# Kernel optimization log

Measured on AMD Instinct MI355X. Metric: run time of the kernel, lower is better.

The kernel has to match this reference:

```python
import jax, jax.numpy as jnp
import numpy as np

VOCAB = 32000
DIM = 1024
HID = 4096
MAXLEN = 2048
NH = 2       # number of sequential LowRankLinearAttention layers
KD = 64      # key_dim hardcoded in the module
B = 2
L = 2048


def setup_inputs() -> dict:
    key = jax.random.key(0)
    ks = jax.random.split(key, 12)
    def rn(k, shape, scale):
        return jax.random.normal(k, shape, dtype=jnp.float32) * scale
    return {
        "input_indices": jax.random.randint(ks[0], (B, L), 0, VOCAB),
        "token_embed": rn(ks[1], (VOCAB, DIM), 0.02),
        "pos_embed": rn(ks[2], (MAXLEN, DIM), 0.02),
        # per-layer attention projections (stored [in, out]; x @ W == torch Linear)
        "Wq": rn(ks[3], (NH, DIM, KD), DIM ** -0.5),
        "Wk": rn(ks[4], (NH, DIM, KD), DIM ** -0.5),
        "Wv": rn(ks[5], (NH, DIM, KD), DIM ** -0.5),
        "Wo": rn(ks[6], (NH, KD, DIM), KD ** -0.5),
        "norm_g": jnp.ones((NH, DIM), jnp.float32),
        "norm_b": jnp.zeros((NH, DIM), jnp.float32),
        "out_norm_g": jnp.ones((DIM,), jnp.float32),
        "out_norm_b": jnp.zeros((DIM,), jnp.float32),
        "W1": rn(ks[7], (DIM, HID), DIM ** -0.5),
        "b1": jnp.zeros((HID,), jnp.float32),
        "W2": rn(ks[8], (HID, VOCAB), HID ** -0.5),
        "b2": jnp.zeros((VOCAB,), jnp.float32),
    }


def _layernorm(x, g, b, eps=1e-5):
    m = jnp.mean(x, axis=-1, keepdims=True)
    v = jnp.var(x, axis=-1, keepdims=True)
    return (x - m) / jnp.sqrt(v + eps) * g + b


def _lowrank_linear_attn(x, Wq, Wk, Wv, Wo):
    # x: [B,L,D]; Q,K,V: [B,L,k]
    Q = jax.nn.elu(x @ Wq) + 1.0
    K = jax.nn.elu(x @ Wk) + 1.0
    V = x @ Wv
    # causal prefix sums of outer products K_t V_t^T -> [B,L,k,k]
    KV_sum = jnp.cumsum(K[..., :, None] * V[..., None, :], axis=1)
    K_sum = jnp.cumsum(K, axis=1)
    num = jnp.einsum('blk,blkj->blj', Q, KV_sum)          # [B,L,k]
    den = jnp.einsum('blk,blk->bl', Q, K_sum)[..., None]  # [B,L,1]
    return (num / (den + 1e-6)) @ Wo


def reference(input_indices, token_embed, pos_embed, Wq, Wk, Wv, Wo,
              norm_g, norm_b, out_norm_g, out_norm_b, W1, b1, W2, b2):
    seq_len = input_indices.shape[1]
    x = token_embed[input_indices] + pos_embed[jnp.arange(seq_len)]
    for i in range(Wq.shape[0]):
        x = x + _lowrank_linear_attn(x, Wq[i], Wk[i], Wv[i], Wo[i])
        x = _layernorm(x, norm_g[i], norm_b[i])
    x = _layernorm(x, out_norm_g, out_norm_b)
    h = jax.nn.gelu(x @ W1 + b1, approximate=False)  # torch nn.GELU default = erf
    logits = h @ W2 + b2
    return logits
```

## Files before the change

### kernel.cpp

```cpp
#include <hip/hip_runtime.h>

typedef __attribute__((ext_vector_type(4))) float  f4;
typedef __attribute__((ext_vector_type(2))) float  f2;
typedef __attribute__((ext_vector_type(4))) unsigned short us4;
typedef __attribute__((ext_vector_type(8))) short  s8;
typedef __attribute__((ext_vector_type(4))) float  f32x4;

__device__ __forceinline__ unsigned short f2bf(float f) {
  unsigned u = __float_as_uint(f);
  u += 0x7fffu + ((u >> 16) & 1u);
  return (unsigned short)(u >> 16);
}
__device__ __forceinline__ float elu1(float x) { return x > 0.f ? x + 1.f : __expf(x); }
__device__ __forceinline__ float gelu_erf(float x) { return 0.5f * x * (1.f + erff(x * 0.70710678118654752f)); }

__device__ __forceinline__ void async16(const void* g, void* l) {
  __builtin_amdgcn_global_load_lds((const __attribute__((address_space(1))) void*)g,
                                   (__attribute__((address_space(3))) void*)l, 16, 0, 0);
}

__device__ __forceinline__ void rawbar() {
  asm volatile("s_barrier" ::: "memory");
}

__device__ __forceinline__ unsigned l2u(const void* p) {
  return (unsigned)(size_t)(const __attribute__((address_space(3))) char*)p;
}
template<int OFF>
__device__ __forceinline__ void dsr(s8& d, unsigned base) {
  asm volatile("ds_read_b128 %0, %1 offset:%2" : "=v"(d) : "v"(base), "i"(OFF));
}
template<int KB>
__device__ __forceinline__ void readA8(s8 (&af)[8], unsigned base) {
  dsr<(0 * 2 + KB) * 1024>(af[0], base);
  dsr<(1 * 2 + KB) * 1024>(af[1], base);
  dsr<(2 * 2 + KB) * 1024>(af[2], base);
  dsr<(3 * 2 + KB) * 1024>(af[3], base);
  dsr<(4 * 2 + KB) * 1024>(af[4], base);
  dsr<(5 * 2 + KB) * 1024>(af[5], base);
  dsr<(6 * 2 + KB) * 1024>(af[6], base);
  dsr<(7 * 2 + KB) * 1024>(af[7], base);
}

__global__ __launch_bounds__(256) void embed_kernel(
    const int* __restrict__ idx, const float* __restrict__ tok,
    const float* __restrict__ pos, float* __restrict__ X, unsigned short* __restrict__ XB)
{
  int g = blockIdx.x * 256 + threadIdx.x;
  int t = g >> 8;
  int c4 = (g & 255) * 4;
  int l = t & 2047;
  int tk = idx[t];
  f4 v = *(const f4*)(tok + (size_t)tk * 1024 + c4);
  f4 p = *(const f4*)(pos + (size_t)l * 1024 + c4);
  v += p;
  *(f4*)(X + (size_t)t * 1024 + c4) = v;
  us4 o = { f2bf(v[0]), f2bf(v[1]), f2bf(v[2]), f2bf(v[3]) };
  *(us4*)(XB + (size_t)t * 1024 + c4) = o;
}

__global__ __launch_bounds__(256) void transpose_cvt(
    const float* __restrict__ src, unsigned short* __restrict__ dst, int N, int K)
{
  __shared__ unsigned short t[64][72];
  int k0 = blockIdx.x * 64, n0 = blockIdx.y * 64;
  int tid = threadIdx.x;
#pragma unroll
  for (int i = 0; i < 4; ++i) {
    int f = tid + i * 256;
    int r = f >> 4, c4 = (f & 15) * 4;
    f4 v = *(const f4*)(src + (size_t)(k0 + r) * N + n0 + c4);
    us4 o = { f2bf(v[0]), f2bf(v[1]), f2bf(v[2]), f2bf(v[3]) };
    *(us4*)&t[r][c4] = o;
  }
  __syncthreads();
#pragma unroll
  for (int i = 0; i < 4; ++i) {
    int f = tid + i * 256;
    int nr = f >> 4, kc4 = (f & 15) * 4;
    us4 o = { t[kc4 + 0][nr], t[kc4 + 1][nr], t[kc4 + 2][nr], t[kc4 + 3][nr] };
    *(us4*)(dst + (size_t)(n0 + nr) * K + k0 + kc4) = o;
  }
}

template<int EPI, int BF32>
__global__ __launch_bounds__(256) void gemm_bt(
    const unsigned short* __restrict__ A, const unsigned short* __restrict__ Bt,
    const float* __restrict__ Bf, const float* __restrict__ bias,
    void* __restrict__ Cv, int M, int N, int K, int mtiles)
{
  __shared__ unsigned short As[128 * 32];
  __shared__ unsigned short Bs[128 * 32];
  int bid = blockIdx.x;
  int mt = bid % mtiles, nt = bid / mtiles;
  int m0 = mt * 128, n0 = nt * 128;
  int tid = threadIdx.x, lane = tid & 63, w = tid >> 6;
  int wm = (w & 1) * 64, wn = (w >> 1) * 64;

  int c0 = w * 128 + lane, c1 = c0 + 64;
  size_t aO0 = (size_t)(m0 + (c0 >> 2)) * K + (size_t)((c0 & 3) * 8);
  size_t aO1 = (size_t)(m0 + (c1 >> 2)) * K + (size_t)((c1 & 3) * 8);
  size_t bO0 = (size_t)(n0 + (c0 >> 2)) * K + (size_t)((c0 & 3) * 8);
  size_t bO1 = (size_t)(n0 + (c1 >> 2)) * K + (size_t)((c1 & 3) * 8);
  unsigned short* lA0 = As + (w * 128) * 8;
  unsigned short* lA1 = As + (w * 128 + 64) * 8;
  unsigned short* lB0 = Bs + (w * 128) * 8;
  unsigned short* lB1 = Bs + (w * 128 + 64) * 8;

  f32x4 acc[4][4];
  f32x4 zz = {0.f, 0.f, 0.f, 0.f};
#pragma unroll
  for (int i = 0; i < 4; ++i)
#pragma unroll
    for (int j = 0; j < 4; ++j) acc[i][j] = zz;

  int rr = lane & 15, kh = (lane >> 4) * 8;
  const unsigned short* Ar = As + (wm + rr) * 32 + kh;
  const unsigned short* Br = Bs + (wn + rr) * 32 + kh;

  for (int k0 = 0; k0 < K; k0 += 32) {
    async16(A + aO0 + k0, lA0);
    async16(A + aO1 + k0, lA1);
    if constexpr (!BF32) {
      async16(Bt + bO0 + k0, lB0);
      async16(Bt + bO1 + k0, lB1);
    } else {
#pragma unroll
      for (int i = 0; i < 4; ++i) {
        int f = tid + i * 256;
        int kr = f >> 5, c4 = (f & 31) * 4;
        f4 v = *(const f4*)(Bf + (size_t)(k0 + kr) * N + n0 + c4);
#pragma unroll
        for (int e = 0; e < 4; ++e) Bs[(c4 + e) * 32 + kr] = f2bf(v[e]);
      }
    }
    __syncthreads();
    s8 af[4], bfr[4];
#pragma unroll
    for (int mi = 0; mi < 4; ++mi) af[mi] = *(const s8*)(Ar + mi * 512);
#pragma unroll
    for (int ni = 0; ni < 4; ++ni) bfr[ni] = *(const s8*)(Br + ni * 512);
#pragma unroll
    for (int mi = 0; mi < 4; ++mi)
#pragma unroll
      for (int ni = 0; ni < 4; ++ni)
        acc[mi][ni] = __builtin_amdgcn_mfma_f32_16x16x32_bf16(af[mi], bfr[ni], acc[mi][ni], 0, 0, 0);
    __syncthreads();
  }

  int cr = (lane >> 4) * 4;
#pragma unroll
  for (int mi = 0; mi < 4; ++mi) {
#pragma unroll
    for (int ni = 0; ni < 4; ++ni) {
      int gc = n0 + wn + ni * 16 + rr;
      float bv = (EPI > 0) ? bias[gc] : 0.f;
#pragma unroll
      for (int r = 0; r < 4; ++r) {
        int gr = m0 + wm + mi * 16 + cr + r;
        float v = acc[mi][ni][r] + bv;
        if constexpr (EPI == 1) {
          ((unsigned short*)Cv)[(size_t)gr * N + gc] = f2bf(gelu_erf(v));
        } else {
          ((float*)Cv)[(size_t)gr * N + gc] = v;
        }
      }
    }
  }
}

template<int RA, int RDKB, int RDNH, int ACCN, typename STG>
__device__ __forceinline__ void phaseX(
    unsigned ArdB, unsigned BrdB,
    s8 (&afDst)[8], s8 (&bfDst)[2],
    const s8 (&afUse)[8], const s8 (&bfUse)[2],
    f32x4 (&acc)[8][4], STG stg)
{
  dsr<((RDNH * 2 + 0) * 2 + RDKB) * 1024>(bfDst[0], BrdB);
  dsr<((RDNH * 2 + 1) * 2 + RDKB) * 1024>(bfDst[1], BrdB);
  if constexpr (RA) readA8<RDKB>(afDst, ArdB);
  stg();
  asm volatile("s_waitcnt vmcnt(6)" ::: "memory");
  rawbar();
  if constexpr (RA) asm volatile("s_waitcnt lgkmcnt(10)" ::: "memory");
  else              asm volatile("s_waitcnt lgkmcnt(2)" ::: "memory");
  __builtin_amdgcn_sched_barrier(0);
  __builtin_amdgcn_s_setprio(1);
#pragma unroll
  for (int f = 0; f < 8; ++f) {
    acc[f][ACCN * 2 + 0] =
        __builtin_amdgcn_mfma_f32_16x16x32_bf16(afUse[f], bfUse[0], acc[f][ACCN * 2 + 0], 0, 0, 0);
    acc[f][ACCN * 2 + 1] =
        __builtin_amdgcn_mfma_f32_16x16x32_bf16(afUse[f], bfUse[1], acc[f][ACCN * 2 + 1], 0, 0, 0);
  }
  __builtin_amdgcn_s_setprio(0);
  __builtin_amdgcn_sched_barrier(0);
}

template<int EPI>
__global__ __launch_bounds__(512, 2) void gemm256(
    const unsigned short* __restrict__ A, const unsigned short* __restrict__ Bt,
    const float* __restrict__ bias, void* __restrict__ Cv,
    int M, int N, int K, int mtiles)
{
  __shared__ __align__(16) char A0r[32768];
  __shared__ __align__(16) char B0r[32768];
  __shared__ __align__(16) char A1r[32768];
  __shared__ __align__(16) char B1r[32768];

  const int tid = threadIdx.x, lane = tid & 63, w = tid >> 6;
  const int wm = w >> 2, wn = w & 3;
  const int NT = K >> 6;

  int nwg = gridDim.x, orig = blockIdx.x;
  int q = nwg >> 3, r = nwg & 7;
  int xcd = orig & 7, lin = orig >> 3;
  int swz = (xcd < r ? xcd * (q + 1) : r * (q + 1) + (xcd - r) * q) + lin;
  int mt = swz % mtiles, nt = swz / mtiles;
  int m0 = mt * 256, n0 = nt * 256;

  const size_t klane8 = (size_t)((lane >> 4) << 3);
  const size_t arow0 = (size_t)(m0 + w * 32 + (lane & 15)) * K;
  const size_t arow1 = arow0 + (size_t)16 * K;
  const size_t brow0 = (size_t)(n0 + w * 32 + (lane & 15)) * K;
  const size_t brow1 = brow0 + (size_t)16 * K;

  auto stgA = [&](char* reg, int kt, int kb) {
    int ktc = kt < NT ? kt : NT - 1;
    size_t kk = (size_t)ktc * 64 + (size_t)(kb * 32) + klane8;
    char* d = reg + w * 4096 + kb * 1024;
    async16(A + arow0 + kk, d);
    async16(A + arow1 + kk, d + 2048);
  };
  auto stgB = [&](char* reg, int kt, int kb) {
    int ktc = kt < NT ? kt : NT - 1;
    size_t kk = (size_t)ktc * 64 + (size_t)(kb * 32) + klane8;
    char* d = reg + w * 4096 + kb * 1024;
    async16(Bt + brow0 + kk, d);
    async16(Bt + brow1 + kk, d + 2048);
  };

  const unsigned AB0 = l2u(A0r + wm * 16384 + lane * 16);
  const unsigned BB0 = l2u(B0r + wn * 8192 + lane * 16);
  const unsigned AB1 = l2u(A1r + wm * 16384 + lane * 16);
  const unsigned BB1 = l2u(B1r + wn * 8192 + lane * 16);

  f32x4 acc[8][4];
  f32x4 zz = {0.f, 0.f, 0.f, 0.f};
#pragma unroll
  for (int i = 0; i < 8; ++i)
#pragma unroll
    for (int j = 0; j < 4; ++j) acc[i][j] = zz;
  s8 afA[8], afB[8], bfA[2], bfB[2];

  stgA(A0r, 0, 0); stgB(B0r, 0, 0);
  stgA(A0r, 0, 1); stgB(B0r, 0, 1);
  stgA(A1r, 1, 0); stgB(B1r, 1, 0);
  asm volatile("s_waitcnt vmcnt(8)" ::: "memory");
  rawbar();
  readA8<0>(afA, AB0);
  dsr<0>(bfA[0], BB0);
  dsr<2048>(bfA[1], BB0);

  for (int te = 0; te < NT; te += 2) {
    phaseX<0, 0, 1, 0>(AB0, BB0, afA, bfB, afA, bfA, acc, [&] { stgA(A1r, te + 1, 1); });
    phaseX<1, 1, 1, 1>(AB0, BB0, afB, bfA, afA, bfB, acc, [&] { stgB(B1r, te + 1, 1); });
    phaseX<0, 1, 0, 1>(AB0, BB0, afA, bfB, afB, bfA, acc, [&] { stgA(A0r, te + 2, 0); });
    phaseX<1, 0, 0, 0>(AB1, BB1, afA, bfA, afB, bfB, acc, [&] { stgB(B0r, te + 2, 0); });
    phaseX<0, 0, 1, 0>(AB1, BB1, afA, bfB, afA, bfA, acc, [&] { stgA(A0r, te + 2, 1); });
    phaseX<1, 1, 1, 1>(AB1, BB1, afB, bfA, afA, bfB, acc, [&] { stgB(B0r, te + 2, 1); });
    phaseX<0, 1, 0, 1>(AB1, BB1, afA, bfB, afB, bfA, acc, [&] { stgA(A1r, te + 3, 0); });
    phaseX<1, 0, 0, 0>(AB0, BB0, afA, bfA, afB, bfB, acc, [&] { stgB(B1r, te + 3, 0); });
  }

  asm volatile("s_waitcnt vmcnt(0) lgkmcnt(0)" ::: "memory");
  __builtin_amdgcn_sched_barrier(0);

  int rr = lane & 15, cr = (lane >> 4) * 4;
#pragma unroll
  for (int f = 0; f < 8; ++f) {
#pragma unroll
    for (int ni = 0; ni < 4; ++ni) {
      int gc = n0 + wn * 64 + ni * 16 + rr;
      float bv = bias[gc];
#pragma unroll
      for (int rg = 0; rg < 4; ++rg) {
        int gr = m0 + wm * 128 + f * 16 + cr + rg;
        float v = acc[f][ni][rg] + bv;
        if constexpr (EPI == 1) {
          ((unsigned short*)Cv)[(size_t)gr * N + gc] = f2bf(gelu_erf(v));
        } else {
          ((float*)Cv)[(size_t)gr * N + gc] = v;
        }
      }
    }
  }
}

__global__ __launch_bounds__(256) void chunk_sums(
    const float* __restrict__ QKV, float* __restrict__ KVc, float* __restrict__ Ksum)
{
  __shared__ float Ks[64][68], Vs[64][68];
  int blk = blockIdx.x, t0 = blk * 64, tid = threadIdx.x;
#pragma unroll
  for (int i = 0; i < 4; ++i) {
    int f = tid + i * 256;
    int r = f >> 4, c4 = (f & 15) * 4;
    const float* s = QKV + (size_t)(t0 + r) * 256;
    f4 k = *(const f4*)(s + 64 + c4);
    f4 v = *(const f4*)(s + 128 + c4);
#pragma unroll
    for (int e = 0; e < 4; ++e) { Ks[r][c4 + e] = elu1(k[e]); Vs[r][c4 + e] = v[e]; }
  }
  __syncthreads();
  int i0 = tid >> 2, jb = (tid & 3) * 16;
  f4 a0 = {0,0,0,0}, a1 = {0,0,0,0}, a2 = {0,0,0,0}, a3 = {0,0,0,0};
  for (int t = 0; t < 64; ++t) {
    float kk = Ks[t][i0];
    a0 += kk * (*(const f4*)&Vs[t][jb]);
    a1 += kk * (*(const f4*)&Vs[t][jb + 4]);
    a2 += kk * (*(const f4*)&Vs[t][jb + 8]);
    a3 += kk * (*(const f4*)&Vs[t][jb + 12]);
  }
  float* d = KVc + (size_t)blk * 4096 + i0 * 64 + jb;
  *(f4*)(d) = a0; *(f4*)(d + 4) = a1; *(f4*)(d + 8) = a2; *(f4*)(d + 12) = a3;
  if (tid < 64) {
    float s = 0.f;
    for (int t = 0; t < 64; ++t) s += Ks[t][tid];
    Ksum[(size_t)blk * 64 + tid] = s;
  }
}

__global__ __launch_bounds__(256) void prefix_state(
    const float* __restrict__ KVc, const float* __restrict__ Ksum,
    float* __restrict__ KVp, float* __restrict__ Ksump)
{
  int b = blockIdx.x >> 3, seg = blockIdx.x & 7;
  int e = seg * 512 + threadIdx.x * 2;
  f2 run = {0.f, 0.f};
#pragma unroll
  for (int c = 0; c < 32; ++c) {
    size_t base = ((size_t)b * 32 + c) * 4096 + e;
    *(f2*)(KVp + base) = run;
    run += *(const f2*)(KVc + base);
  }
  if (seg == 0 && threadIdx.x < 64) {
    float rs = 0.f; int i = threadIdx.x;
#pragma unroll
    for (int c = 0; c < 32; ++c) {
      size_t base = ((size_t)b * 32 + c) * 64 + i;
      Ksump[base] = rs;
      rs += Ksum[base];
    }
  }
}

__global__ __launch_bounds__(256) void attn_ns(
    const float* __restrict__ QKV, const float* __restrict__ KVp,
    const float* __restrict__ Ksump, float* __restrict__ NsG)
{
  __shared__ float Qs[64][68], Ks[64][68], Vs[64][68], Ss[64][68], Ps[64][68];
  __shared__ float ksps[64];
  int blk = blockIdx.x, t0 = blk * 64, tid = threadIdx.x;
#pragma unroll
  for (int i = 0; i < 4; ++i) {
    int f = tid + i * 256;
    int r = f >> 4, c4 = (f & 15) * 4;
    const float* s = QKV + (size_t)(t0 + r) * 256;
    f4 q = *(const f4*)(s + c4);
    f4 k = *(const f4*)(s + 64 + c4);
    f4 v = *(const f4*)(s + 128 + c4);
    f4 p = *(const f4*)(KVp + (size_t)blk * 4096 + r * 64 + c4);
#pragma unroll
    for (int e = 0; e < 4; ++e) {
      Qs[r][c4 + e] = elu1(q[e]); Ks[r][c4 + e] = elu1(k[e]);
      Vs[r][c4 + e] = v[e];       Ps[r][c4 + e] = p[e];
    }
  }
  if (tid < 64) ksps[tid] = Ksump[(size_t)blk * 64 + tid];
  __syncthreads();
  int tq = tid >> 2, jb = (tid & 3) * 16;
#pragma unroll
  for (int jj = 0; jj < 16; ++jj) {
    int tk = jb + jj;
    float s = 0.f;
    if (tk <= tq) {
#pragma unroll
      for (int k4 = 0; k4 < 16; ++k4) {
        f4 q = *(const f4*)&Qs[tq][k4 * 4];
        f4 k = *(const f4*)&Ks[tk][k4 * 4];
        s += q[0] * k[0] + q[1] * k[1] + q[2] * k[2] + q[3] * k[3];
      }
    }
    Ss[tq][tk] = s;
  }
  __syncthreads();
  f4 a0 = {0,0,0,0}, a1 = {0,0,0,0}, a2 = {0,0,0,0}, a3 = {0,0,0,0};
  for (int t = 0; t < 64; ++t) {
    float s = Ss[tq][t];
    a0 += s * (*(const f4*)&Vs[t][jb]);
    a1 += s * (*(const f4*)&Vs[t][jb + 4]);
    a2 += s * (*(const f4*)&Vs[t][jb + 8]);
    a3 += s * (*(const f4*)&Vs[t][jb + 12]);
  }
  for (int k = 0; k < 64; ++k) {
    float q = Qs[tq][k];
    a0 += q * (*(const f4*)&Ps[k][jb]);
    a1 += q * (*(const f4*)&Ps[k][jb + 4]);
    a2 += q * (*(const f4*)&Ps[k][jb + 8]);
    a3 += q * (*(const f4*)&Ps[k][jb + 12]);
  }
  float den = 0.f;
  for (int t = 0; t < 64; ++t) den += Ss[tq][t];
  for (int k = 0; k < 64; ++k) den += Qs[tq][k] * ksps[k];
  float inv = 1.f / (den + 1e-6f);
  float* d = NsG + (size_t)(t0 + tq) * 64 + jb;
  *(f4*)(d)      = a0 * inv;
  *(f4*)(d + 4)  = a1 * inv;
  *(f4*)(d + 8)  = a2 * inv;
  *(f4*)(d + 12) = a3 * inv;
}

__global__ __launch_bounds__(256) void attn_apply(
    const float* __restrict__ NsG, const float* __restrict__ Wo, float* __restrict__ X)
{
  __shared__ float Ns[64][68];
  __shared__ float Wt[64][260];
  int chunk = blockIdx.x >> 2, dg = blockIdx.x & 3;
  int t0 = chunk * 64, d0 = dg * 256, tid = threadIdx.x;
#pragma unroll
  for (int i = 0; i < 4; ++i) {
    int f = tid + i * 256;
    int r = f >> 4, c4 = (f & 15) * 4;
    *(f4*)&Ns[r][c4] = *(const f4*)(NsG + (size_t)(t0 + r) * 64 + c4);
  }
#pragma unroll
  for (int i = 0; i < 16; ++i) {
    int f = tid + i * 256;
    int r = f >> 6, c4 = (f & 63) * 4;
    *(f4*)&Wt[r][c4] = *(const f4*)(Wo + (size_t)r * 1024 + d0 + c4);
  }
  __syncthreads();
  int w = tid >> 6, lane = tid & 63;
  for (int ts = 0; ts < 16; ++ts) {
    int t = w * 16 + ts;
    float a0 = 0.f, a1 = 0.f, a2 = 0.f, a3 = 0.f;
#pragma unroll
    for (int j = 0; j < 64; ++j) {
      float nv = Ns[t][j];
      a0 += nv * Wt[j][lane];
      a1 += nv * Wt[j][64 + lane];
      a2 += nv * Wt[j][128 + lane];
      a3 += nv * Wt[j][192 + lane];
    }
    size_t o = (size_t)(t0 + t) * 1024 + d0 + lane;
    X[o]       += a0;
    X[o + 64]  += a1;
    X[o + 128] += a2;
    X[o + 192] += a3;
  }
}

__global__ __launch_bounds__(256) void layernorm_kernel(
    float* __restrict__ X, unsigned short* __restrict__ XB,
    const float* __restrict__ g, const float* __restrict__ b)
{
  int t = blockIdx.x * 4 + (threadIdx.x >> 6);
  int lane = threadIdx.x & 63;
  float* row = X + (size_t)t * 1024;
  f4 v[4];
  float s = 0.f, s2 = 0.f;
#pragma unroll
  for (int i = 0; i < 4; ++i) {
    v[i] = *(const f4*)(row + (i * 64 + lane) * 4);
#pragma unroll
    for (int e = 0; e < 4; ++e) { s += v[i][e]; s2 += v[i][e] * v[i][e]; }
  }
#pragma unroll
  for (int off = 32; off > 0; off >>= 1) {
    s  += __shfl_xor(s, off, 64);
    s2 += __shfl_xor(s2, off, 64);
  }
  float mean = s * (1.f / 1024.f);
  float var = s2 * (1.f / 1024.f) - mean * mean;
  float rstd = rsqrtf(var + 1e-5f);
#pragma unroll
  for (int i = 0; i < 4; ++i) {
    int d = (i * 64 + lane) * 4;
    f4 gv = *(const f4*)(g + d);
    f4 bv = *(const f4*)(b + d);
    f4 y;
#pragma unroll
    for (int e = 0; e < 4; ++e) y[e] = (v[i][e] - mean) * rstd * gv[e] + bv[e];
    *(f4*)(row + d) = y;
    us4 o = { f2bf(y[0]), f2bf(y[1]), f2bf(y[2]), f2bf(y[3]) };
    *(us4*)(XB + (size_t)t * 1024 + d) = o;
  }
}

extern "C" void kernel_launch(void* const* d_in, const int* in_sizes, int n_in,
                              void* d_out, int out_size, void* d_ws, size_t ws_size,
                              hipStream_t stream) {
  (void)in_sizes; (void)n_in; (void)out_size;
  const int*   idx = (const int*)d_in[0];
  const float* tok = (const float*)d_in[1];
  const float* pos = (const float*)d_in[2];
  const float* Wq  = (const float*)d_in[3];
  const float* Wk  = (const float*)d_in[4];
  const float* Wv  = (const float*)d_in[5];
  const float* Wo  = (const float*)d_in[6];
  const float* ng  = (const float*)d_in[7];
  const float* nb  = (const float*)d_in[8];
  const float* ong = (const float*)d_in[9];
  const float* onb = (const float*)d_in[10];
  const float* W1  = (const float*)d_in[11];
  const float* b1  = (const float*)d_in[12];
  const float* W2  = (const float*)d_in[13];
  const float* b2  = (const float*)d_in[14];
  float* out = (float*)d_out;
  char* ws = (char*)d_ws;

  float* X            = (float*)(ws + 0);
  unsigned short* XB  = (unsigned short*)(ws + 16777216);
  unsigned short* QT0 = (unsigned short*)(ws + 25165824);
  unsigned short* QT1 = (unsigned short*)(ws + 25690112);
  float* QKVB         = (float*)(ws + 26214400);
  float* KVC          = (float*)(ws + 30408704);
  float* KSUM         = (float*)(ws + 31457280);
  float* KVP          = (float*)(ws + 31490048);
  float* KSP          = (float*)(ws + 32538624);
  unsigned short* W1T = (unsigned short*)(ws + 32571392);
  unsigned short* H   = (unsigned short*)(ws + 40960000);
  unsigned short* W2T = (unsigned short*)(ws + 74514432);
  float* NSG = KVC;
  bool bigws = ws_size >= 336658432ull;

  hipMemsetAsync(QT0, 0, 524288, stream);
  hipMemsetAsync(QT1, 0, 524288, stream);
  transpose_cvt<<<dim3(16, 1), 256, 0, stream>>>(Wq,          QT0,              64, 1024);
  transpose_cvt<<<dim3(16, 1), 256, 0, stream>>>(Wk,          QT0 + 64 * 1024,  64, 1024);
  transpose_cvt<<<dim3(16, 1), 256, 0, stream>>>(Wv,          QT0 + 128 * 1024, 64, 1024);
  transpose_cvt<<<dim3(16, 1), 256, 0, stream>>>(Wq + 65536,  QT1,              64, 1024);
  transpose_cvt<<<dim3(16, 1), 256, 0, stream>>>(Wk + 65536,  QT1 + 64 * 1024,  64, 1024);
  transpose_cvt<<<dim3(16, 1), 256, 0, stream>>>(Wv + 65536,  QT1 + 128 * 1024, 64, 1024);
  transpose_cvt<<<dim3(16, 64), 256, 0, stream>>>(W1, W1T, 4096, 1024);
  if (bigws)
    transpose_cvt<<<dim3(64, 500), 256, 0, stream>>>(W2, W2T, 32000, 4096);

  embed_kernel<<<4096, 256, 0, stream>>>(idx, tok, pos, X, XB);

  for (int layer = 0; layer < 2; ++layer) {
    const unsigned short* QT = layer ? QT1 : QT0;
    gemm_bt<0, 0><<<64, 256, 0, stream>>>(XB, QT, nullptr, nullptr, QKVB, 4096, 256, 1024, 32);
    chunk_sums<<<64, 256, 0, stream>>>(QKVB, KVC, KSUM);
    prefix_state<<<16, 256, 0, stream>>>(KVC, KSUM, KVP, KSP);
    attn_ns<<<64, 256, 0, stream>>>(QKVB, KVP, KSP, NSG);
    attn_apply<<<256, 256, 0, stream>>>(NSG, Wo + (size_t)layer * 65536, X);
    layernorm_kernel<<<1024, 256, 0, stream>>>(X, XB, ng + layer * 1024, nb + layer * 1024);
  }
  layernorm_kernel<<<1024, 256, 0, stream>>>(X, XB, ong, onb);

  gemm256<1><<<256, 512, 0, stream>>>(XB, W1T, b1, H, 4096, 4096, 1024, 16);
  if (bigws)
    gemm256<2><<<2000, 512, 0, stream>>>(H, W2T, b2, out, 4096, 32000, 4096, 16);
  else
    gemm_bt<2, 1><<<8000, 256, 0, stream>>>(H, nullptr, W2, b2, out, 4096, 32000, 4096, 32);
}
```

Measured before the change: 1.654 ms.

## Add 128x128-tile pipelined MFMA GEMM for the vocab projection

Adds a new gemm128 kernel that uses 128x128 output tiles, 4 waves, double-buffered async global-to-LDS staging and bf16 MFMA. The 4096x32000x4096 logits GEMM uses it in place of the 256x256-tile gemm256. The aim is more workgroups (8000 instead of 2000) and two blocks per CU for better occupancy and less wave-quantization tail. The smaller tiles lower arithmetic intensity and add more global and LDS traffic per FLOP.

After: 2.531 ms. +53.0%, slower.

```diff
diff --git a/kernel.cpp b/kernel.cpp
--- a/kernel.cpp
+++ b/kernel.cpp
@@ -287,6 +287,145 @@
       for (int rg = 0; rg < 4; ++rg) {
         int gr = m0 + wm * 128 + f * 16 + cr + rg;
         float v = acc[f][ni][rg] + bv;
+        if constexpr (EPI == 1) {
+          ((unsigned short*)Cv)[(size_t)gr * N + gc] = f2bf(gelu_erf(v));
+        } else {
+          ((float*)Cv)[(size_t)gr * N + gc] = v;
+        }
+      }
+    }
+  }
+}
+
+template<int KB, typename STG>
+__device__ __forceinline__ void phaseY(
+    unsigned AB, unsigned BB, f32x4 (&acc)[4][4], STG stg)
+{
+  s8 a0, a1, a2, a3, b0, b1, b2, b3;
+  dsr<(0 * 2 + KB) * 1024>(a0, AB);
+  dsr<(1 * 2 + KB) * 1024>(a1, AB);
+  dsr<(2 * 2 + KB) * 1024>(a2, AB);
+  dsr<(3 * 2 + KB) * 1024>(a3, AB);
+  dsr<(0 * 2 + KB) * 1024>(b0, BB);
+  dsr<(1 * 2 + KB) * 1024>(b1, BB);
+  dsr<(2 * 2 + KB) * 1024>(b2, BB);
+  dsr<(3 * 2 + KB) * 1024>(b3, BB);
+  stg();
+  asm volatile("s_waitcnt vmcnt(8)" ::: "memory");
+  rawbar();
+  asm volatile("s_waitcnt lgkmcnt(0)" ::: "memory");
+  __builtin_amdgcn_sched_barrier(0);
+  __builtin_amdgcn_s_setprio(1);
+  acc[0][0] = __builtin_amdgcn_mfma_f32_16x16x32_bf16(a0, b0, acc[0][0], 0, 0, 0);
+  acc[1][0] = __builtin_amdgcn_mfma_f32_16x16x32_bf16(a1, b0, acc[1][0], 0, 0, 0);
+  acc[2][0] = __builtin_amdgcn_mfma_f32_16x16x32_bf16(a2, b0, acc[2][0], 0, 0, 0);
+  acc[3][0] = __builtin_amdgcn_mfma_f32_16x16x32_bf16(a3, b0, acc[3][0], 0, 0, 0);
+  acc[0][1] = __builtin_amdgcn_mfma_f32_16x16x32_bf16(a0, b1, acc[0][1], 0, 0, 0);
+  acc[1][1] = __builtin_amdgcn_mfma_f32_16x16x32_bf16(a1, b1, acc[1][1], 0, 0, 0);
+  acc[2][1] = __builtin_amdgcn_mfma_f32_16x16x32_bf16(a2, b1, acc[2][1], 0, 0, 0);
+  acc[3][1] = __builtin_amdgcn_mfma_f32_16x16x32_bf16(a3, b1, acc[3][1], 0, 0, 0);
+  acc[0][2] = __builtin_amdgcn_mfma_f32_16x16x32_bf16(a0, b2, acc[0][2], 0, 0, 0);
+  acc[1][2] = __builtin_amdgcn_mfma_f32_16x16x32_bf16(a1, b2, acc[1][2], 0, 0, 0);
+  acc[2][2] = __builtin_amdgcn_mfma_f32_16x16x32_bf16(a2, b2, acc[2][2], 0, 0, 0);
+  acc[3][2] = __builtin_amdgcn_mfma_f32_16x16x32_bf16(a3, b2, acc[3][2], 0, 0, 0);
+  acc[0][3] = __builtin_amdgcn_mfma_f32_16x16x32_bf16(a0, b3, acc[0][3], 0, 0, 0);
+  acc[1][3] = __builtin_amdgcn_mfma_f32_16x16x32_bf16(a1, b3, acc[1][3], 0, 0, 0);
+  acc[2][3] = __builtin_amdgcn_mfma_f32_16x16x32_bf16(a2, b3, acc[2][3], 0, 0, 0);
+  acc[3][3] = __builtin_amdgcn_mfma_f32_16x16x32_bf16(a3, b3, acc[3][3], 0, 0, 0);
+  __builtin_amdgcn_s_setprio(0);
+  __builtin_amdgcn_sched_barrier(0);
+  rawbar();
+}
+
+template<int EPI>
+__global__ __launch_bounds__(256, 2) void gemm128(
+    const unsigned short* __restrict__ A, const unsigned short* __restrict__ Bt,
+    const float* __restrict__ bias, void* __restrict__ Cv,
+    int M, int N, int K, int mtiles)
+{
+  __shared__ __align__(16) char A0r[16384];
+  __shared__ __align__(16) char B0r[16384];
+  __shared__ __align__(16) char A1r[16384];
+  __shared__ __align__(16) char B1r[16384];
+
+  const int tid = threadIdx.x, lane = tid & 63, w = tid >> 6;
+  const int wm = w >> 1, wn = w & 1;
+  const int NT = K >> 6;
+
+  int nwg = gridDim.x, orig = blockIdx.x;
+  int q = nwg >> 3, r = nwg & 7;
+  int xcd = orig & 7, lin = orig >> 3;
+  int swz = (xcd < r ? xcd * (q + 1) : r * (q + 1) + (xcd - r) * q) + lin;
+  int mt = swz % mtiles, nt = swz / mtiles;
+  int m0 = mt * 128, n0 = nt * 128;
+
+  const int lrow = lane & 15;
+  const size_t lcol = (size_t)((lane >> 4) << 3);
+
+  auto stgA = [&](char* reg, int kt, int kb) {
+    int ktc = kt < NT ? kt : NT - 1;
+    size_t cb = (size_t)ktc * 64 + (size_t)(kb * 32) + lcol;
+#pragma unroll
+    for (int j = 0; j < 2; ++j) {
+      int idx = w * 2 + j;
+      int half = idx >> 2, sub = idx & 3;
+      size_t row = (size_t)(m0 + half * 64 + sub * 16 + lrow);
+      char* d = reg + half * 8192 + (sub * 2 + kb) * 1024;
+      async16(A + row * K + cb, d);
+    }
+  };
+  auto stgB = [&](char* reg, int kt, int kb) {
+    int ktc = kt < NT ? kt : NT - 1;
+    size_t cb = (size_t)ktc * 64 + (size_t)(kb * 32) + lcol;
+#pragma unroll
+    for (int j = 0; j < 2; ++j) {
+      int idx = w * 2 + j;
+      int half = idx >> 2, sub = idx & 3;
+      size_t row = (size_t)(n0 + half * 64 + sub * 16 + lrow);
+      char* d = reg + half * 8192 + (sub * 2 + kb) * 1024;
+      async16(Bt + row * K + cb, d);
+    }
+  };
+
+  const unsigned AB0 = l2u(A0r + wm * 8192 + lane * 16);
+  const unsigned BB0 = l2u(B0r + wn * 8192 + lane * 16);
+  const unsigned AB1 = l2u(A1r + wm * 8192 + lane * 16);
+  const unsigned BB1 = l2u(B1r + wn * 8192 + lane * 16);
+
+  f32x4 acc[4][4];
+  f32x4 zz = {0.f, 0.f, 0.f, 0.f};
+#pragma unroll
+  for (int i = 0; i < 4; ++i)
+#pragma unroll
+    for (int j = 0; j < 4; ++j) acc[i][j] = zz;
+
+  stgA(A0r, 0, 0); stgB(B0r, 0, 0);
+  stgA(A0r, 0, 1); stgB(B0r, 0, 1);
+  stgA(A1r, 1, 0); stgB(B1r, 1, 0);
+  asm volatile("s_waitcnt vmcnt(8)" ::: "memory");
+  rawbar();
+
+  for (int te = 0; te < NT; te += 2) {
+    phaseY<0>(AB0, BB0, acc, [&] { stgA(A1r, te + 1, 1); stgB(B1r, te + 1, 1); });
+    phaseY<1>(AB0, BB0, acc, [&] { stgA(A0r, te + 2, 0); stgB(B0r, te + 2, 0); });
+    phaseY<0>(AB1, BB1, acc, [&] { stgA(A0r, te + 2, 1); stgB(B0r, te + 2, 1); });
+    phaseY<1>(AB1, BB1, acc, [&] { stgA(A1r, te + 3, 0); stgB(B1r, te + 3, 0); });
+  }
+
+  asm volatile("s_waitcnt vmcnt(0) lgkmcnt(0)" ::: "memory");
+  __builtin_amdgcn_sched_barrier(0);
+
+  int rr = lane & 15, cr = (lane >> 4) * 4;
+#pragma unroll
+  for (int mi = 0; mi < 4; ++mi) {
+#pragma unroll
+    for (int ni = 0; ni < 4; ++ni) {
+      int gc = n0 + wn * 64 + ni * 16 + rr;
+      float bv = bias[gc];
+#pragma unroll
+      for (int rg = 0; rg < 4; ++rg) {
+        int gr = m0 + wm * 64 + mi * 16 + cr + rg;
+        float v = acc[mi][ni][rg] + bv;
         if constexpr (EPI == 1) {
           ((unsigned short*)Cv)[(size_t)gr * N + gc] = f2bf(gelu_erf(v));
         } else {
@@ -562,7 +701,7 @@
 
   gemm256<1><<<256, 512, 0, stream>>>(XB, W1T, b1, H, 4096, 4096, 1024, 16);
   if (bigws)
-    gemm256<2><<<2000, 512, 0, stream>>>(H, W2T, b2, out, 4096, 32000, 4096, 16);
+    gemm128<2><<<8000, 256, 0, stream>>>(H, W2T, b2, out, 4096, 32000, 4096, 32);
   else
     gemm_bt<2, 1><<<8000, 256, 0, stream>>>(H, nullptr, W2, b2, out, 4096, 32000, 4096, 32);
 }
```

## Switch big GEMM to 1024-thread blocks with 64x64 warp tiles

Applied to the files above, without the earlier changes.

Replaces the 512-thread 256x256 GEMM, where each warp computes 128x64 with software-pipelined register fragments, by a 1024-thread version. Each of the 16 warps now computes a 64x64 subtile and reloads its A/B fragments from LDS every phase, with an extra barrier per phase. The goal is more waves per CU to hide latency and a simpler phase schedule. In exchange, each MFMA does less register-level reuse, LDS read traffic per FLOP rises, and occupancy is limited to one 1024-thread block per CU given the 128KB of LDS.

Result: slower. 1.702 ms (+2.9%).

```diff
diff --git a/kernel.cpp b/kernel.cpp
--- a/kernel.cpp
+++ b/kernel.cpp
@@ -29,17 +29,6 @@
 template<int OFF>
 __device__ __forceinline__ void dsr(s8& d, unsigned base) {
   asm volatile("ds_read_b128 %0, %1 offset:%2" : "=v"(d) : "v"(base), "i"(OFF));
-}
-template<int KB>
-__device__ __forceinline__ void readA8(s8 (&af)[8], unsigned base) {
-  dsr<(0 * 2 + KB) * 1024>(af[0], base);
-  dsr<(1 * 2 + KB) * 1024>(af[1], base);
-  dsr<(2 * 2 + KB) * 1024>(af[2], base);
-  dsr<(3 * 2 + KB) * 1024>(af[3], base);
-  dsr<(4 * 2 + KB) * 1024>(af[4], base);
-  dsr<(5 * 2 + KB) * 1024>(af[5], base);
-  dsr<(6 * 2 + KB) * 1024>(af[6], base);
-  dsr<(7 * 2 + KB) * 1024>(af[7], base);
 }
 
 __global__ __launch_bounds__(256) void embed_kernel(
@@ -169,36 +158,48 @@
   }
 }
 
-template<int RA, int RDKB, int RDNH, int ACCN, typename STG>
-__device__ __forceinline__ void phaseX(
-    unsigned ArdB, unsigned BrdB,
-    s8 (&afDst)[8], s8 (&bfDst)[2],
-    const s8 (&afUse)[8], const s8 (&bfUse)[2],
-    f32x4 (&acc)[8][4], STG stg)
-{
-  dsr<((RDNH * 2 + 0) * 2 + RDKB) * 1024>(bfDst[0], BrdB);
-  dsr<((RDNH * 2 + 1) * 2 + RDKB) * 1024>(bfDst[1], BrdB);
-  if constexpr (RA) readA8<RDKB>(afDst, ArdB);
+template<int KB, typename STG>
+__device__ __forceinline__ void phaseZ(
+    unsigned AB, unsigned BB, f32x4 (&acc)[4][4], STG stg)
+{
+  s8 a0, a1, a2, a3, b0, b1, b2, b3;
+  dsr<(0 * 2 + KB) * 1024>(a0, AB);
+  dsr<(1 * 2 + KB) * 1024>(a1, AB);
+  dsr<(2 * 2 + KB) * 1024>(a2, AB);
+  dsr<(3 * 2 + KB) * 1024>(a3, AB);
+  dsr<(0 * 2 + KB) * 1024>(b0, BB);
+  dsr<(1 * 2 + KB) * 1024>(b1, BB);
+  dsr<(2 * 2 + KB) * 1024>(b2, BB);
+  dsr<(3 * 2 + KB) * 1024>(b3, BB);
   stg();
-  asm volatile("s_waitcnt vmcnt(6)" ::: "memory");
+  asm volatile("s_waitcnt vmcnt(4)" ::: "memory");
   rawbar();
-  if constexpr (RA) asm volatile("s_waitcnt lgkmcnt(10)" ::: "memory");
-  else              asm volatile("s_waitcnt lgkmcnt(2)" ::: "memory");
+  asm volatile("s_waitcnt lgkmcnt(0)" ::: "memory");
   __builtin_amdgcn_sched_barrier(0);
   __builtin_amdgcn_s_setprio(1);
-#pragma unroll
-  for (int f = 0; f < 8; ++f) {
-    acc[f][ACCN * 2 + 0] =
-        __builtin_amdgcn_mfma_f32_16x16x32_bf16(afUse[f], bfUse[0], acc[f][ACCN * 2 + 0], 0, 0, 0);
-    acc[f][ACCN * 2 + 1] =
-        __builtin_amdgcn_mfma_f32_16x16x32_bf16(afUse[f], bfUse[1], acc[f][ACCN * 2 + 1], 0, 0, 0);
-  }
+  acc[0][0] = __builtin_amdgcn_mfma_f32_16x16x32_bf16(a0, b0, acc[0][0], 0, 0, 0);
+  acc[1][0] = __builtin_amdgcn_mfma_f32_16x16x32_bf16(a1, b0, acc[1][0], 0, 0, 0);
+  acc[2][0] = __builtin_amdgcn_mfma_f32_16x16x32_bf16(a2, b0, acc[2][0], 0, 0, 0);
+  acc[3][0] = __builtin_amdgcn_mfma_f32_16x16x32_bf16(a3, b0, acc[3][0], 0, 0, 0);
+  acc[0][1] = __builtin_amdgcn_mfma_f32_16x16x32_bf16(a0, b1, acc[0][1], 0, 0, 0);
+  acc[1][1] = __builtin_amdgcn_mfma_f32_16x16x32_bf16(a1, b1, acc[1][1], 0, 0, 0);
+  acc[2][1] = __builtin_amdgcn_mfma_f32_16x16x32_bf16(a2, b1, acc[2][1], 0, 0, 0);
+  acc[3][1] = __builtin_amdgcn_mfma_f32_16x16x32_bf16(a3, b1, acc[3][1], 0, 0, 0);
+  acc[0][2] = __builtin_amdgcn_mfma_f32_16x16x32_bf16(a0, b2, acc[0][2], 0, 0, 0);
+  acc[1][2] = __builtin_amdgcn_mfma_f32_16x16x32_bf16(a1, b2, acc[1][2], 0, 0, 0);
+  acc[2][2] = __builtin_amdgcn_mfma_f32_16x16x32_bf16(a2, b2, acc[2][2], 0, 0, 0);
+  acc[3][2] = __builtin_amdgcn_mfma_f32_16x16x32_bf16(a3, b2, acc[3][2], 0, 0, 0);
+  acc[0][3] = __builtin_amdgcn_mfma_f32_16x16x32_bf16(a0, b3, acc[0][3], 0, 0, 0);
+  acc[1][3] = __builtin_amdgcn_mfma_f32_16x16x32_bf16(a1, b3, acc[1][3], 0, 0, 0);
+  acc[2][3] = __builtin_amdgcn_mfma_f32_16x16x32_bf16(a2, b3, acc[2][3], 0, 0, 0);
+  acc[3][3] = __builtin_amdgcn_mfma_f32_16x16x32_bf16(a3, b3, acc[3][3], 0, 0, 0);
   __builtin_amdgcn_s_setprio(0);
   __builtin_amdgcn_sched_barrier(0);
+  rawbar();
 }
 
 template<int EPI>
-__global__ __launch_bounds__(512, 2) void gemm256(
+__global__ __launch_bounds__(1024) void gemm1k(
     const unsigned short* __restrict__ A, const unsigned short* __restrict__ Bt,
     const float* __restrict__ bias, void* __restrict__ Cv,
     int M, int N, int K, int mtiles)
@@ -219,58 +220,41 @@
   int mt = swz % mtiles, nt = swz / mtiles;
   int m0 = mt * 256, n0 = nt * 256;
 
-  const size_t klane8 = (size_t)((lane >> 4) << 3);
-  const size_t arow0 = (size_t)(m0 + w * 32 + (lane & 15)) * K;
-  const size_t arow1 = arow0 + (size_t)16 * K;
-  const size_t brow0 = (size_t)(n0 + w * 32 + (lane & 15)) * K;
-  const size_t brow1 = brow0 + (size_t)16 * K;
+  const unsigned short* aP = A + (size_t)(m0 + w * 16 + (lane & 15)) * K + ((lane >> 4) << 3);
+  const unsigned short* bP = Bt + (size_t)(n0 + w * 16 + (lane & 15)) * K + ((lane >> 4) << 3);
 
   auto stgA = [&](char* reg, int kt, int kb) {
     int ktc = kt < NT ? kt : NT - 1;
-    size_t kk = (size_t)ktc * 64 + (size_t)(kb * 32) + klane8;
-    char* d = reg + w * 4096 + kb * 1024;
-    async16(A + arow0 + kk, d);
-    async16(A + arow1 + kk, d + 2048);
+    async16(aP + ktc * 64 + kb * 32, reg + w * 2048 + kb * 1024);
   };
   auto stgB = [&](char* reg, int kt, int kb) {
     int ktc = kt < NT ? kt : NT - 1;
-    size_t kk = (size_t)ktc * 64 + (size_t)(kb * 32) + klane8;
-    char* d = reg + w * 4096 + kb * 1024;
-    async16(Bt + brow0 + kk, d);
-    async16(Bt + brow1 + kk, d + 2048);
+    async16(bP + ktc * 64 + kb * 32, reg + w * 2048 + kb * 1024);
   };
 
-  const unsigned AB0 = l2u(A0r + wm * 16384 + lane * 16);
+  const unsigned AB0 = l2u(A0r + wm * 8192 + lane * 16);
   const unsigned BB0 = l2u(B0r + wn * 8192 + lane * 16);
-  const unsigned AB1 = l2u(A1r + wm * 16384 + lane * 16);
+  const unsigned AB1 = l2u(A1r + wm * 8192 + lane * 16);
   const unsigned BB1 = l2u(B1r + wn * 8192 + lane * 16);
 
-  f32x4 acc[8][4];
+  f32x4 acc[4][4];
   f32x4 zz = {0.f, 0.f, 0.f, 0.f};
 #pragma unroll
-  for (int i = 0; i < 8; ++i)
+  for (int i = 0; i < 4; ++i)
 #pragma unroll
     for (int j = 0; j < 4; ++j) acc[i][j] = zz;
-  s8 afA[8], afB[8], bfA[2], bfB[2];
 
   stgA(A0r, 0, 0); stgB(B0r, 0, 0);
   stgA(A0r, 0, 1); stgB(B0r, 0, 1);
   stgA(A1r, 1, 0); stgB(B1r, 1, 0);
-  asm volatile("s_waitcnt vmcnt(8)" ::: "memory");
+  asm volatile("s_waitcnt vmcnt(4)" ::: "memory");
   rawbar();
-  readA8<0>(afA, AB0);
-  dsr<0>(bfA[0], BB0);
-  dsr<2048>(bfA[1], BB0);
 
   for (int te = 0; te < NT; te += 2) {
-    phaseX<0, 0, 1, 0>(AB0, BB0, afA, bfB, afA, bfA, acc, [&] { stgA(A1r, te + 1, 1); });
-    phaseX<1, 1, 1, 1>(AB0, BB0, afB, bfA, afA, bfB, acc, [&] { stgB(B1r, te + 1, 1); });
-    phaseX<0, 1, 0, 1>(AB0, BB0, afA, bfB, afB, bfA, acc, [&] { stgA(A0r, te + 2, 0); });
-    phaseX<1, 0, 0, 0>(AB1, BB1, afA, bfA, afB, bfB, acc, [&] { stgB(B0r, te + 2, 0); });
-    phaseX<0, 0, 1, 0>(AB1, BB1, afA, bfB, afA, bfA, acc, [&] { stgA(A0r, te + 2, 1); });
-    phaseX<1, 1, 1, 1>(AB1, BB1, afB, bfA, afA, bfB, acc, [&] { stgB(B0r, te + 2, 1); });
-    phaseX<0, 1, 0, 1>(AB1, BB1, afA, bfB, afB, bfA, acc, [&] { stgA(A1r, te + 3, 0); });
-    phaseX<1, 0, 0, 0>(AB0, BB0, afA, bfA, afB, bfB, acc, [&] { stgB(B1r, te + 3, 0); });
+    phaseZ<0>(AB0, BB0, acc, [&] { stgA(A1r, te + 1, 1); stgB(B1r, te + 1, 1); });
+    phaseZ<1>(AB0, BB0, acc, [&] { stgA(A0r, te + 2, 0); stgB(B0r, te + 2, 0); });
+    phaseZ<0>(AB1, BB1, acc, [&] { stgA(A0r, te + 2, 1); stgB(B0r, te + 2, 1); });
+    phaseZ<1>(AB1, BB1, acc, [&] { stgA(A1r, te + 3, 0); stgB(B1r, te + 3, 0); });
   }
 
   asm volatile("s_waitcnt vmcnt(0) lgkmcnt(0)" ::: "memory");
@@ -278,15 +262,15 @@
 
   int rr = lane & 15, cr = (lane >> 4) * 4;
 #pragma unroll
-  for (int f = 0; f < 8; ++f) {
+  for (int mi = 0; mi < 4; ++mi) {
 #pragma unroll
     for (int ni = 0; ni < 4; ++ni) {
       int gc = n0 + wn * 64 + ni * 16 + rr;
       float bv = bias[gc];
 #pragma unroll
       for (int rg = 0; rg < 4; ++rg) {
-        int gr = m0 + wm * 128 + f * 16 + cr + rg;
-        float v = acc[f][ni][rg] + bv;
+        int gr = m0 + wm * 64 + mi * 16 + cr + rg;
+        float v = acc[mi][ni][rg] + bv;
         if constexpr (EPI == 1) {
           ((unsigned short*)Cv)[(size_t)gr * N + gc] = f2bf(gelu_erf(v));
         } else {
@@ -560,9 +544,9 @@
   }
   layernorm_kernel<<<1024, 256, 0, stream>>>(X, XB, ong, onb);
 
-  gemm256<1><<<256, 512, 0, stream>>>(XB, W1T, b1, H, 4096, 4096, 1024, 16);
+  gemm1k<1><<<256, 1024, 0, stream>>>(XB, W1T, b1, H, 4096, 4096, 1024, 16);
   if (bigws)
-    gemm256<2><<<2000, 512, 0, stream>>>(H, W2T, b2, out, 4096, 32000, 4096, 16);
+    gemm1k<2><<<2000, 1024, 0, stream>>>(H, W2T, b2, out, 4096, 32000, 4096, 16);
   else
     gemm_bt<2, 1><<<8000, 256, 0, stream>>>(H, nullptr, W2, b2, out, 4096, 32000, 4096, 32);
 }
```

## Simplify large GEMM main loop to per-tile read-compute-stage and reroute W1 GEMM

Applied to the files above, without the earlier changes.

Replaces the eight-phase interleaved LDS-read/MFMA ping-pong schedule in the 256-tile GEMM with a simpler loop. Each iteration reads all A/B fragments for a K tile, runs the MFMAs in four groups gated by staggered lgkmcnt waits, then issues async loads for tile t+2 and barriers. The min-blocks occupancy hint is dropped, and the W1 GEMM is moved to the smaller gemm_bt kernel. The aim is fewer scheduling constraints and less register juggling. In exchange, LDS reads overlap less with MFMA work, register use for fragments grows, and there is no barrier between the last fragment reads and the overwrite of the same LDS buffer.

Result: faster. 1.599 ms (-3.4%).

```diff
diff --git a/kernel.cpp b/kernel.cpp
--- a/kernel.cpp
+++ b/kernel.cpp
@@ -29,17 +29,6 @@
 template<int OFF>
 __device__ __forceinline__ void dsr(s8& d, unsigned base) {
   asm volatile("ds_read_b128 %0, %1 offset:%2" : "=v"(d) : "v"(base), "i"(OFF));
-}
-template<int KB>
-__device__ __forceinline__ void readA8(s8 (&af)[8], unsigned base) {
-  dsr<(0 * 2 + KB) * 1024>(af[0], base);
-  dsr<(1 * 2 + KB) * 1024>(af[1], base);
-  dsr<(2 * 2 + KB) * 1024>(af[2], base);
-  dsr<(3 * 2 + KB) * 1024>(af[3], base);
-  dsr<(4 * 2 + KB) * 1024>(af[4], base);
-  dsr<(5 * 2 + KB) * 1024>(af[5], base);
-  dsr<(6 * 2 + KB) * 1024>(af[6], base);
-  dsr<(7 * 2 + KB) * 1024>(af[7], base);
 }
 
 __global__ __launch_bounds__(256) void embed_kernel(
@@ -169,36 +158,8 @@
   }
 }
 
-template<int RA, int RDKB, int RDNH, int ACCN, typename STG>
-__device__ __forceinline__ void phaseX(
-    unsigned ArdB, unsigned BrdB,
-    s8 (&afDst)[8], s8 (&bfDst)[2],
-    const s8 (&afUse)[8], const s8 (&bfUse)[2],
-    f32x4 (&acc)[8][4], STG stg)
-{
-  dsr<((RDNH * 2 + 0) * 2 + RDKB) * 1024>(bfDst[0], BrdB);
-  dsr<((RDNH * 2 + 1) * 2 + RDKB) * 1024>(bfDst[1], BrdB);
-  if constexpr (RA) readA8<RDKB>(afDst, ArdB);
-  stg();
-  asm volatile("s_waitcnt vmcnt(6)" ::: "memory");
-  rawbar();
-  if constexpr (RA) asm volatile("s_waitcnt lgkmcnt(10)" ::: "memory");
-  else              asm volatile("s_waitcnt lgkmcnt(2)" ::: "memory");
-  __builtin_amdgcn_sched_barrier(0);
-  __builtin_amdgcn_s_setprio(1);
-#pragma unroll
-  for (int f = 0; f < 8; ++f) {
-    acc[f][ACCN * 2 + 0] =
-        __builtin_amdgcn_mfma_f32_16x16x32_bf16(afUse[f], bfUse[0], acc[f][ACCN * 2 + 0], 0, 0, 0);
-    acc[f][ACCN * 2 + 1] =
-        __builtin_amdgcn_mfma_f32_16x16x32_bf16(afUse[f], bfUse[1], acc[f][ACCN * 2 + 1], 0, 0, 0);
-  }
-  __builtin_amdgcn_s_setprio(0);
-  __builtin_amdgcn_sched_barrier(0);
-}
-
 template<int EPI>
-__global__ __launch_bounds__(512, 2) void gemm256(
+__global__ __launch_bounds__(512) void gemm2(
     const unsigned short* __restrict__ A, const unsigned short* __restrict__ Bt,
     const float* __restrict__ bias, void* __restrict__ Cv,
     int M, int N, int K, int mtiles)
@@ -251,26 +212,99 @@
   for (int i = 0; i < 8; ++i)
 #pragma unroll
     for (int j = 0; j < 4; ++j) acc[i][j] = zz;
-  s8 afA[8], afB[8], bfA[2], bfB[2];
-
-  stgA(A0r, 0, 0); stgB(B0r, 0, 0);
-  stgA(A0r, 0, 1); stgB(B0r, 0, 1);
-  stgA(A1r, 1, 0); stgB(B1r, 1, 0);
+
+  stgA(A0r, 0, 0); stgA(A0r, 0, 1); stgB(B0r, 0, 0); stgB(B0r, 0, 1);
+  stgA(A1r, 1, 0); stgA(A1r, 1, 1); stgB(B1r, 1, 0); stgB(B1r, 1, 1);
   asm volatile("s_waitcnt vmcnt(8)" ::: "memory");
   rawbar();
-  readA8<0>(afA, AB0);
-  dsr<0>(bfA[0], BB0);
-  dsr<2048>(bfA[1], BB0);
-
-  for (int te = 0; te < NT; te += 2) {
-    phaseX<0, 0, 1, 0>(AB0, BB0, afA, bfB, afA, bfA, acc, [&] { stgA(A1r, te + 1, 1); });
-    phaseX<1, 1, 1, 1>(AB0, BB0, afB, bfA, afA, bfB, acc, [&] { stgB(B1r, te + 1, 1); });
-    phaseX<0, 1, 0, 1>(AB0, BB0, afA, bfB, afB, bfA, acc, [&] { stgA(A0r, te + 2, 0); });
-    phaseX<1, 0, 0, 0>(AB1, BB1, afA, bfA, afB, bfB, acc, [&] { stgB(B0r, te + 2, 0); });
-    phaseX<0, 0, 1, 0>(AB1, BB1, afA, bfB, afA, bfA, acc, [&] { stgA(A0r, te + 2, 1); });
-    phaseX<1, 1, 1, 1>(AB1, BB1, afB, bfA, afA, bfB, acc, [&] { stgB(B0r, te + 2, 1); });
-    phaseX<0, 1, 0, 1>(AB1, BB1, afA, bfB, afB, bfA, acc, [&] { stgA(A1r, te + 3, 0); });
-    phaseX<1, 0, 0, 0>(AB0, BB0, afA, bfA, afB, bfB, acc, [&] { stgB(B1r, te + 3, 0); });
+
+  for (int t = 0; t < NT; ++t) {
+    const int odd = t & 1;
+    const unsigned AB = odd ? AB1 : AB0;
+    const unsigned BB = odd ? BB1 : BB0;
+    char* Ad = odd ? A1r : A0r;
+    char* Bd = odd ? B1r : B0r;
+
+    s8 bf[8], af[16];
+    dsr<(0 * 2 + 0) * 1024>(bf[0], BB);
+    dsr<(0 * 2 + 1) * 1024>(bf[1], BB);
+    dsr<(1 * 2 + 0) * 1024>(bf[2], BB);
+    dsr<(1 * 2 + 1) * 1024>(bf[3], BB);
+    dsr<(2 * 2 + 0) * 1024>(bf[4], BB);
+    dsr<(2 * 2 + 1) * 1024>(bf[5], BB);
+    dsr<(3 * 2 + 0) * 1024>(bf[6], BB);
+    dsr<(3 * 2 + 1) * 1024>(bf[7], BB);
+    dsr<(0 * 2 + 0) * 1024>(af[0], AB);
+    dsr<(0 * 2 + 1) * 1024>(af[1], AB);
+    dsr<(1 * 2 + 0) * 1024>(af[2], AB);
+    dsr<(1 * 2 + 1) * 1024>(af[3], AB);
+    dsr<(2 * 2 + 0) * 1024>(af[4], AB);
+    dsr<(2 * 2 + 1) * 1024>(af[5], AB);
+    dsr<(3 * 2 + 0) * 1024>(af[6], AB);
+    dsr<(3 * 2 + 1) * 1024>(af[7], AB);
+    dsr<(4 * 2 + 0) * 1024>(af[8], AB);
+    dsr<(4 * 2 + 1) * 1024>(af[9], AB);
+    dsr<(5 * 2 + 0) * 1024>(af[10], AB);
+    dsr<(5 * 2 + 1) * 1024>(af[11], AB);
+    dsr<(6 * 2 + 0) * 1024>(af[12], AB);
+    dsr<(6 * 2 + 1) * 1024>(af[13], AB);
+    dsr<(7 * 2 + 0) * 1024>(af[14], AB);
+    dsr<(7 * 2 + 1) * 1024>(af[15], AB);
+
+    asm volatile("s_waitcnt lgkmcnt(12)" ::: "memory");
+    __builtin_amdgcn_sched_barrier(0);
+    __builtin_amdgcn_s_setprio(1);
+#pragma unroll
+    for (int ni = 0; ni < 4; ++ni) {
+#pragma unroll
+      for (int f = 0; f < 2; ++f) {
+        acc[f][ni] = __builtin_amdgcn_mfma_f32_16x16x32_bf16(af[f * 2 + 0], bf[ni * 2 + 0], acc[f][ni], 0, 0, 0);
+        acc[f][ni] = __builtin_amdgcn_mfma_f32_16x16x32_bf16(af[f * 2 + 1], bf[ni * 2 + 1], acc[f][ni], 0, 0, 0);
+      }
+    }
+    __builtin_amdgcn_s_setprio(0);
+    asm volatile("s_waitcnt lgkmcnt(8)" ::: "memory");
+    __builtin_amdgcn_sched_barrier(0);
+    __builtin_amdgcn_s_setprio(1);
+#pragma unroll
+    for (int ni = 0; ni < 4; ++ni) {
+#pragma unroll
+      for (int f = 2; f < 4; ++f) {
+        acc[f][ni] = __builtin_amdgcn_mfma_f32_16x16x32_bf16(af[f * 2 + 0], bf[ni * 2 + 0], acc[f][ni], 0, 0, 0);
+        acc[f][ni] = __builtin_amdgcn_mfma_f32_16x16x32_bf16(af[f * 2 + 1], bf[ni * 2 + 1], acc[f][ni], 0, 0, 0);
+      }
+    }
+    __builtin_amdgcn_s_setprio(0);
+    asm volatile("s_waitcnt lgkmcnt(4)" ::: "memory");
+    __builtin_amdgcn_sched_barrier(0);
+    __builtin_amdgcn_s_setprio(1);
+#pragma unroll
+    for (int ni = 0; ni < 4; ++ni) {
+#pragma unroll
+      for (int f = 4; f < 6; ++f) {
+        acc[f][ni] = __builtin_amdgcn_mfma_f32_16x16x32_bf16(af[f * 2 + 0], bf[ni * 2 + 0], acc[f][ni], 0, 0, 0);
+        acc[f][ni] = __builtin_amdgcn_mfma_f32_16x16x32_bf16(af[f * 2 + 1], bf[ni * 2 + 1], acc[f][ni], 0, 0, 0);
+      }
+    }
+    __builtin_amdgcn_s_setprio(0);
+    asm volatile("s_waitcnt lgkmcnt(0)" ::: "memory");
+    __builtin_amdgcn_sched_barrier(0);
+    __builtin_amdgcn_s_setprio(1);
+#pragma unroll
+    for (int ni = 0; ni < 4; ++ni) {
+#pragma unroll
+      for (int f = 6; f < 8; ++f) {
+        acc[f][ni] = __builtin_amdgcn_mfma_f32_16x16x32_bf16(af[f * 2 + 0], bf[ni * 2 + 0], acc[f][ni], 0, 0, 0);
+        acc[f][ni] = __builtin_amdgcn_mfma_f32_16x16x32_bf16(af[f * 2 + 1], bf[ni * 2 + 1], acc[f][ni], 0, 0, 0);
+      }
+    }
+    __builtin_amdgcn_s_setprio(0);
+    __builtin_amdgcn_sched_barrier(0);
+
+    stgA(Ad, t + 2, 0); stgA(Ad, t + 2, 1);
+    stgB(Bd, t + 2, 0); stgB(Bd, t + 2, 1);
+    asm volatile("s_waitcnt vmcnt(8)" ::: "memory");
+    rawbar();
   }
 
   asm volatile("s_waitcnt vmcnt(0) lgkmcnt(0)" ::: "memory");
@@ -560,9 +594,9 @@
   }
   layernorm_kernel<<<1024, 256, 0, stream>>>(X, XB, ong, onb);
 
-  gemm256<1><<<256, 512, 0, stream>>>(XB, W1T, b1, H, 4096, 4096, 1024, 16);
+  gemm_bt<1, 0><<<1024, 256, 0, stream>>>(XB, W1T, nullptr, b1, H, 4096, 4096, 1024, 32);
   if (bigws)
-    gemm256<2><<<2000, 512, 0, stream>>>(H, W2T, b2, out, 4096, 32000, 4096, 16);
+    gemm2<2><<<2000, 512, 0, stream>>>(H, W2T, b2, out, 4096, 32000, 4096, 16);
   else
     gemm_bt<2, 1><<<8000, 256, 0, stream>>>(H, nullptr, W2, b2, out, 4096, 32000, 4096, 32);
 }
```
